# Kernel optimization log

Hardware: AMD Instinct MI355X
Metric: run time of the kernel (lower is better)

The kernel has to match this reference:

```python
import jax, jax.numpy as jnp
import numpy as np

VOCAB, EMB, NDIM, B, T = 50000, 300, 512, 128, 128


def gru_cell(x, h, Wih, Whh, bih, bhh):
    # torch nn.GRU gate order: [r, z, n]
    gi = x @ Wih.T + bih
    gh = h @ Whh.T + bhh
    i_r, i_z, i_n = jnp.split(gi, 3, axis=-1)
    h_r, h_z, h_n = jnp.split(gh, 3, axis=-1)
    r = jax.nn.sigmoid(i_r + h_r)
    z = jax.nn.sigmoid(i_z + h_z)
    n = jnp.tanh(i_n + r * h_n)
    return (1.0 - z) * n + z * h


def masked_gru(X, mask, h0, Wih, Whh, bih, bhh):
    # X: T x B x d, mask: T x B, h0: B x n. Replicates _gru_forward:
    # step-0 output is stored UNmasked (o_tm1 is None), later steps blend.
    h_raw = gru_cell(X[0], h0, Wih, Whh, bih, bhh)
    m0 = mask[0][:, None]
    h = h_raw * m0 + h0 * (1.0 - m0)
    o = h_raw

    def step(carry, inp):
        h, o = carry
        x_t, m_t = inp
        m = m_t[:, None]
        hr = gru_cell(x_t, h, Wih, Whh, bih, bhh)
        h_new = hr * m + h * (1.0 - m)
        o_new = hr * m + o * (1.0 - m)
        return (h_new, o_new), o_new

    (h_f, _), o_rest = jax.lax.scan(step, (h, o), (X[1:], mask[1:]))
    return jnp.concatenate([o[None], o_rest], axis=0), h_f


def rte_forward(premise, hypothesis, E, p_Wih, p_Whh, p_bih, p_bhh,
                h_Wih, h_Whh, h_bih, h_bhh, m_Wih, m_Whh, m_bih, m_bhh,
                W_y, W_h, W_r, W_alpha, out_W, out_b):
    bsz = premise.shape[0]
    n_dim = W_y.shape[0]
    mask_p = (premise != 0).astype(E.dtype).T            # T x B
    mask_h = (hypothesis != 0).astype(E.dtype).T
    enc_p = E[premise].transpose(1, 0, 2)                # T x B x EMB (eval: no dropout)
    enc_h = E[hypothesis].transpose(1, 0, 2)
    h0 = jnp.zeros((bsz, n_dim), dtype=E.dtype)
    o_p, h_n = masked_gru(enc_p, mask_p, h0, p_Wih, p_Whh, p_bih, p_bhh)
    o_h, _ = masked_gru(enc_h, mask_h, h_n, h_Wih, h_Whh, h_bih, h_bhh)

    Y = o_p.transpose(1, 0, 2)                           # B x Tp x n
    Yw = Y @ W_y                                         # hoisted: constant across steps
    maskY = mask_p.T                                     # B x Tp

    def step(r, inp):
        h_t, m_t = inp
        s = h_t @ W_h + r @ W_r                          # B x n
        M = jnp.tanh(Yw + s[:, None, :])                 # B x Tp x n
        alpha = (M @ W_alpha)[..., 0]                    # B x Tp
        alpha = alpha - 1000.0 * (1.0 - maskY)
        alpha = jax.nn.softmax(alpha, axis=-1)
        a = jnp.einsum('bt,btn->bn', alpha, Y)
        m_in = jnp.concatenate([a, h_t], axis=-1)        # B x 2n
        rr = gru_cell(m_in, r, m_Wih, m_Whh, m_bih, m_bhh)
        m = m_t[:, None]
        r_new = rr * m + r * (1.0 - m)
        return r_new, alpha

    r0 = jnp.zeros((bsz, n_dim), dtype=E.dtype)
    r_f, _alpha_vec = jax.lax.scan(step, r0, (o_h, mask_h))
    logits = r_f @ out_W.T + out_b                       # B x 3
    return jax.nn.log_softmax(logits, axis=-1)


def setup_inputs():
    key = jax.random.key(0)
    ks = jax.random.split(key, 22)
    s = 0.05
    def rn(k, sh):
        return jax.random.normal(k, sh, dtype=jnp.float32) * s
    G = 3 * NDIM
    return {
        "premise": jax.random.randint(ks[0], (B, T), 0, VOCAB),
        "hypothesis": jax.random.randint(ks[1], (B, T), 0, VOCAB),
        "E": rn(ks[2], (VOCAB, EMB)),
        "p_Wih": rn(ks[3], (G, EMB)), "p_Whh": rn(ks[4], (G, NDIM)),
        "p_bih": rn(ks[5], (G,)), "p_bhh": rn(ks[6], (G,)),
        "h_Wih": rn(ks[7], (G, EMB)), "h_Whh": rn(ks[8], (G, NDIM)),
        "h_bih": rn(ks[9], (G,)), "h_bhh": rn(ks[10], (G,)),
        "m_Wih": rn(ks[11], (G, 2 * NDIM)), "m_Whh": rn(ks[12], (G, NDIM)),
        "m_bih": rn(ks[13], (G,)), "m_bhh": rn(ks[14], (G,)),
        "W_y": rn(ks[15], (NDIM, NDIM)), "W_h": rn(ks[16], (NDIM, NDIM)),
        "W_r": rn(ks[17], (NDIM, NDIM)), "W_alpha": rn(ks[18], (NDIM, 1)),
        "out_W": rn(ks[19], (3, NDIM)), "out_b": rn(ks[20], (3,)),
    }


def reference(premise, hypothesis, E, p_Wih, p_Whh, p_bih, p_bhh,
              h_Wih, h_Whh, h_bih, h_bhh, m_Wih, m_Whh, m_bih, m_bhh,
              W_y, W_h, W_r, W_alpha, out_W, out_b):
    return rte_forward(premise, hypothesis, E, p_Wih, p_Whh, p_bih, p_bhh,
                       h_Wih, h_Whh, h_bih, h_bhh, m_Wih, m_Whh, m_bih, m_bhh,
                       W_y, W_h, W_r, W_alpha, out_W, out_b)
```

## Files before the change

### kernel.cpp

```cpp
#include <hip/hip_runtime.h>
#include <math.h>

#define B_SZ 128
#define T_SZ 128
#define EMBD 300
#define ND 512
#define G3 1536
#define FPAD 32
#define NFID 320
#define NREP 8

typedef short s16x8 __attribute__((ext_vector_type(8)));
typedef float f32x4 __attribute__((ext_vector_type(4)));
typedef unsigned long long u64;

__device__ __forceinline__ unsigned short f2b(float x) {
    unsigned u = __float_as_uint(x);
    unsigned r = (u + 0x7fff + ((u >> 16) & 1)) >> 16;
    return (unsigned short)r;
}
__device__ __forceinline__ float b2f(unsigned short v) {
    return __uint_as_float(((unsigned)v) << 16);
}
__device__ __forceinline__ float fsigmoid(float x) { return 1.0f / (1.0f + __expf(-x)); }
__device__ __forceinline__ float ftanh(float x) { return 1.0f - 2.0f / (__expf(2.0f * x) + 1.0f); }

__device__ __forceinline__ f32x4 mfma16(s16x8 a, s16x8 b, f32x4 c) {
    return __builtin_amdgcn_mfma_f32_16x16x32_bf16(a, b, c, 0, 0, 0);
}

__device__ __forceinline__ u64 cld64(const void* p) {
    return __hip_atomic_load((const u64*)p, __ATOMIC_RELAXED, __HIP_MEMORY_SCOPE_AGENT);
}
__device__ __forceinline__ void cst64(void* p, u64 v) {
    __hip_atomic_store((u64*)p, v, __ATOMIC_RELAXED, __HIP_MEMORY_SCOPE_AGENT);
}
__device__ __forceinline__ unsigned cld32(const void* p) {
    return __hip_atomic_load((const unsigned*)p, __ATOMIC_RELAXED, __HIP_MEMORY_SCOPE_AGENT);
}
__device__ __forceinline__ void cst32(void* p, unsigned v) {
    __hip_atomic_store((unsigned*)p, v, __ATOMIC_RELAXED, __HIP_MEMORY_SCOPE_AGENT);
}
__device__ __forceinline__ s16x8 cld_frag(const unsigned short* p) {
    union { u64 q[2]; s16x8 v; } u;
    u.q[0] = cld64(p);
    u.q[1] = cld64(p + 4);
    return u.v;
}

__device__ __forceinline__ void postflag(unsigned* flags, int base, int id, unsigned ep)
{
    if (threadIdx.x < NREP)
        cst32(&flags[((long)threadIdx.x * NFID + base + id) * FPAD], ep);
}
__device__ __forceinline__ void waitflags(const unsigned* flags, int base, int n,
                                          unsigned ep, int rep)
{
    const unsigned* fr = flags + (long)rep * NFID * FPAD;
    if (threadIdx.x < 64) {
#pragma unroll 1
        for (int i = threadIdx.x; i < n; i += 64)
            while (cld32(&fr[(long)(base + i) * FPAD]) < ep)
                __builtin_amdgcn_s_sleep(2);
    }
    __syncthreads();
}
__device__ __forceinline__ void fbar(unsigned* flags, int base, int nb, unsigned ep)
{
    __syncthreads();
    postflag(flags, base, blockIdx.x & 63, ep);
    waitflags(flags, base, nb, ep, blockIdx.x & 7);
}

#define FB_GRUP 0
#define FB_GRUH 64
#define FB_LF   128
#define FB_UF   256
#define FB_SF   288

template<typename AT, bool OB>
__global__ __launch_bounds__(256)
void mfma_gemm(const AT* __restrict__ A, const int* __restrict__ idxA,
               const unsigned short* __restrict__ Wb, const float* __restrict__ bias,
               void* __restrict__ Cv,
               int M, int N, int K, int ldA, int Kpad, int ldC, int permC)
{
    __shared__ unsigned short As[64][40];
    __shared__ unsigned short Bs[64][40];
    const int tid = threadIdx.x;
    const int wv = tid >> 6, lane = tid & 63;
    const int wm = wv >> 1, wn = wv & 1;
    const int m0 = blockIdx.y * 64, n0 = blockIdx.x * 64;

    f32x4 acc[2][2] = {{{0.f,0.f,0.f,0.f},{0.f,0.f,0.f,0.f}},
                       {{0.f,0.f,0.f,0.f},{0.f,0.f,0.f,0.f}}};
    const int r_st = tid >> 2, k_st = (tid & 3) * 8;

    long arow = -1;
    {
        int gm = m0 + r_st;
        if (gm < M) arow = idxA ? (long)idxA[gm] : (long)gm;
    }

    const int kIters = (K + 31) / 32;
    for (int it = 0; it < kIters; ++it) {
        const int kg = it * 32 + k_st;
        {
            s16x8 pk = {0,0,0,0,0,0,0,0};
            if (arow >= 0) {
                if constexpr (sizeof(AT) == 2) {
                    if (kg + 8 <= K) {
                        pk = *(const s16x8*)((const unsigned short*)A + arow * (long)ldA + kg);
                    } else {
#pragma unroll
                        for (int j = 0; j < 8; ++j)
                            if (kg + j < K) pk[j] = (short)((const unsigned short*)A)[arow * (long)ldA + kg + j];
                    }
                } else {
                    if (kg + 8 <= K) {
                        const float* p = (const float*)A + arow * (long)ldA + kg;
                        f32x4 u0 = *(const f32x4*)p;
                        f32x4 u1 = *(const f32x4*)(p + 4);
#pragma unroll
                        for (int j = 0; j < 4; ++j) { pk[j] = (short)f2b(u0[j]); pk[4+j] = (short)f2b(u1[j]); }
                    } else {
#pragma unroll
                        for (int j = 0; j < 8; ++j) {
                            int kk = kg + j;
                            if (kk < K) pk[j] = (short)f2b(((const float*)A)[arow * (long)ldA + kk]);
                        }
                    }
                }
            }
            *(s16x8*)&As[r_st][k_st] = pk;
        }
        {
            int gn = n0 + r_st;
            s16x8 pk = {0,0,0,0,0,0,0,0};
            if (gn < N) pk = *(const s16x8*)&Wb[(long)gn * Kpad + kg];
            *(s16x8*)&Bs[r_st][k_st] = pk;
        }
        __syncthreads();
        {
            const int koff = (lane >> 4) * 8;
            s16x8 af[2], bfr[2];
#pragma unroll
            for (int f = 0; f < 2; ++f) {
                af[f]  = *(s16x8*)&As[wm * 32 + f * 16 + (lane & 15)][koff];
                bfr[f] = *(s16x8*)&Bs[wn * 32 + f * 16 + (lane & 15)][koff];
            }
#pragma unroll
            for (int fi = 0; fi < 2; ++fi)
#pragma unroll
                for (int fj = 0; fj < 2; ++fj)
                    acc[fi][fj] = mfma16(af[fi], bfr[fj], acc[fi][fj]);
        }
        __syncthreads();
    }
#pragma unroll
    for (int fi = 0; fi < 2; ++fi)
#pragma unroll
        for (int fj = 0; fj < 2; ++fj)
#pragma unroll
            for (int r = 0; r < 4; ++r) {
                int m = m0 + wm * 32 + fi * 16 + (lane >> 4) * 4 + r;
                int n = n0 + wn * 32 + fj * 16 + (lane & 15);
                if (m < M && n < N) {
                    float v = acc[fi][fj][r];
                    if (bias) v += bias[n];
                    long mo = permC ? ((long)(m & 127) * B_SZ + (m >> 7)) : (long)m;
                    if constexpr (OB) ((unsigned short*)Cv)[mo * ldC + n] = f2b(v);
                    else               ((float*)Cv)[mo * ldC + n] = v;
                }
            }
}

#define GRU_NB 64
__global__ __launch_bounds__(256, 1)
void gru_chain(const unsigned short* __restrict__ Whh_b, const float* __restrict__ GI,
               const float* __restrict__ bhh, const int* __restrict__ toks,
               float* __restrict__ h32,
               unsigned short* __restrict__ h16a, unsigned short* __restrict__ h16b,
               unsigned short* __restrict__ o_bt,
               unsigned* __restrict__ flags, int fbase)
{
    __shared__ unsigned short wlds[3][16][512];
    __shared__ unsigned short ht[64][20];
    const int tid = threadIdx.x;
    const int wv = tid >> 6, lane = tid & 63;
    const int dt = blockIdx.x & 31, bh = blockIdx.x >> 5;
    const int b0 = bh * 64;

    for (int s = 0; s < 12; ++s) {
        int slot = tid + s * 256;
        int g = slot >> 10, rem = slot & 1023, ks = rem >> 6, ln = rem & 63;
        int row = g * ND + dt * 16 + (ln & 15);
        int k = ks * 32 + (ln >> 4) * 8;
        *(s16x8*)&wlds[g][ks][ln * 8] = *(const s16x8*)&Whh_b[(long)row * ND + k];
    }
    __syncthreads();

    const int d = dt * 16 + (lane & 15);
    const int brow = b0 + wv * 16 + (lane >> 4) * 4;
    const int arow = b0 + wv * 16 + (lane & 15);
    const int akoff = (lane >> 4) * 8;

    float hreg[4];
#pragma unroll
    for (int rr = 0; rr < 4; ++rr) hreg[rr] = h32[(long)(brow + rr) * ND + d];

    float o_run[4] = {0.f, 0.f, 0.f, 0.f};
    unsigned ep = 0;

    for (int t = 0; t < T_SZ; ++t) {
        const unsigned short* hin16 = (t & 1) ? h16b : h16a;
        unsigned short* hout16 = (t & 1) ? h16a : h16b;

        const float* git = GI + (long)t * (B_SZ * G3);
        float gi_r[4], gi_z[4], gi_n[4]; int mk[4];
#pragma unroll
        for (int rr = 0; rr < 4; ++rr) {
            int b = brow + rr;
            gi_r[rr] = git[(long)b * G3 + d];
            gi_z[rr] = git[(long)b * G3 + ND + d];
            gi_n[rr] = git[(long)b * G3 + 2 * ND + d];
            mk[rr]   = toks[b * T_SZ + t];
        }

        f32x4 acc0 = {0,0,0,0}, acc1 = {0,0,0,0}, acc2 = {0,0,0,0};
#pragma unroll
        for (int ks = 0; ks < 16; ++ks) {
            s16x8 a  = cld_frag(&hin16[(long)arow * ND + ks * 32 + akoff]);
            s16x8 br = *(s16x8*)&wlds[0][ks][lane * 8];
            s16x8 bz = *(s16x8*)&wlds[1][ks][lane * 8];
            s16x8 bn = *(s16x8*)&wlds[2][ks][lane * 8];
            acc0 = mfma16(a, br, acc0);
            acc1 = mfma16(a, bz, acc1);
            acc2 = mfma16(a, bn, acc2);
        }

#pragma unroll
        for (int rr = 0; rr < 4; ++rr) {
            int b = brow + rr;
            float rg = fsigmoid(gi_r[rr] + acc0[rr] + bhh[d]);
            float zg = fsigmoid(gi_z[rr] + acc1[rr] + bhh[ND + d]);
            float ng = ftanh(gi_n[rr] + rg * (acc2[rr] + bhh[2 * ND + d]));
            float hr = (1.0f - zg) * ng + zg * hreg[rr];
            bool m = mk[rr] != 0;
            float hn = m ? hr : hreg[rr];
            hreg[rr] = hn;
            ht[b - b0][lane & 15] = f2b(hn);
            if (t == T_SZ - 1) h32[(long)b * ND + d] = hn;
            o_run[rr] = (t == 0) ? hr : (m ? hr : o_run[rr]);
            o_bt[((long)b * T_SZ + t) * ND + d] = f2b(o_run[rr]);
        }
        __syncthreads();
        {
            int bl = tid & 63, dq = tid >> 6;
            u64 v = *(u64*)&ht[bl][dq * 4];
            cst64(&hout16[(long)(b0 + bl) * ND + dt * 16 + dq * 4], v);
        }
        fbar(flags, fbase, GRU_NB, ++ep);
    }
}

#define UP_NB 32
#define YPITCH 536
__global__ __launch_bounds__(256, 1)
void match_chain(const unsigned short* __restrict__ WrT_b,
                 const unsigned short* __restrict__ mWihL_b,
                 const unsigned short* __restrict__ mWhh_b,
                 const unsigned short* __restrict__ OHWh_tb,
                 const unsigned short* __restrict__ OHGI_tb,
                 const float* __restrict__ m_bhh, const float* __restrict__ Walpha,
                 const unsigned short* __restrict__ Yw_bb,
                 const unsigned short* __restrict__ Y_bb,
                 const int* __restrict__ prem, const int* __restrict__ hyp,
                 float* __restrict__ r32,
                 unsigned short* __restrict__ r16a, unsigned short* __restrict__ r16b,
                 unsigned short* __restrict__ a16, unsigned short* __restrict__ s16,
                 unsigned* __restrict__ flags)
{
    __shared__ __align__(16) unsigned char smem[157696];
    const int tid = threadIdx.x;
    const int wv = tid >> 6, lane = tid & 63;

    if (blockIdx.x < 128) {
        const int b = blockIdx.x;
        const int rep = b & 7;
        unsigned short (*ywl)[YPITCH] = (unsigned short(*)[YPITCH])smem;
        float* wal  = (float*)(smem + 137216);
        float* sarr = (float*)(smem + 139264);
        float* part = (float*)(smem + 141312);
        float* lg   = (float*)(smem + 142336);
        float* red  = (float*)(smem + 142848);
        float* sr2  = (float*)(smem + 142880);

        for (int s = 0; s < 32; ++s) {
            int c = s * 256 + tid;
            int row = c >> 6, cg = c & 63;
            *(s16x8*)&ywl[row][cg * 8] =
                *(const s16x8*)&Yw_bb[((long)b * T_SZ + row) * ND + cg * 8];
        }
        if (tid < 128) {
            f32x4 w = *(const f32x4*)&Walpha[tid * 4];
            *(f32x4*)&wal[tid * 4] = w;
        }
        float mmreg = 0.f;
        if (tid < 128) mmreg = (prem[b * T_SZ + tid] != 0) ? 0.f : 1000.f;
        __syncthreads();

        const int tp = tid >> 1, gh = tid & 1;
        const unsigned short* yrow = &ywl[tp][gh * 256];
        const float* sp  = &sarr[gh * 256];
        const float* wap = &wal[gh * 256];
        const int g = tid >> 7, lt = tid & 127, n4 = lt * 4;

        for (int t = 0; t < T_SZ; ++t) {
            waitflags(flags, FB_SF, UP_NB, (unsigned)(t + 1), rep);
            if (tid < 64) {
                s16x8 q = cld_frag(&s16[(long)b * ND + tid * 8]);
#pragma unroll
                for (int j = 0; j < 8; ++j) sarr[tid * 8 + j] = b2f((unsigned short)q[j]);
            }
            __syncthreads();
            {
                float acc = 0.f;
#pragma unroll 4
                for (int i8 = 0; i8 < 32; ++i8) {
                    s16x8 yw = *(const s16x8*)&yrow[i8 * 8];
                    f32x4 s0 = *(const f32x4*)&sp[i8 * 8];
                    f32x4 s1 = *(const f32x4*)&sp[i8 * 8 + 4];
                    f32x4 w0 = *(const f32x4*)&wap[i8 * 8];
                    f32x4 w1 = *(const f32x4*)&wap[i8 * 8 + 4];
#pragma unroll
                    for (int j = 0; j < 4; ++j)
                        acc += ftanh(b2f((unsigned short)yw[j]) + s0[j]) * w0[j];
#pragma unroll
                    for (int j = 0; j < 4; ++j)
                        acc += ftanh(b2f((unsigned short)yw[4 + j]) + s1[j]) * w1[j];
                }
                part[tid] = acc;
            }
            __syncthreads();
            if (tid < 128) lg[tid] = __expf(part[tid * 2] + part[tid * 2 + 1] - mmreg);
            __syncthreads();
            float suml = 0.f;
            f32x4 acw = {0.f, 0.f, 0.f, 0.f};
#pragma unroll 8
            for (int i = 0; i < 64; ++i) {
                int tpp = g * 64 + i;
                float al = lg[tpp];
                suml += al;
                u64 q = *(const u64*)&Y_bb[((long)b * T_SZ + tpp) * ND + n4];
                acw[0] += al * b2f((unsigned short)q);
                acw[1] += al * b2f((unsigned short)(q >> 16));
                acw[2] += al * b2f((unsigned short)(q >> 32));
                acw[3] += al * b2f((unsigned short)(q >> 48));
            }
            if (g == 1) {
                *(f32x4*)&sr2[n4] = acw;
                if (lt == 0) red[0] = suml;
            }
            __syncthreads();
            if (g == 0) {
                float inv = 1.0f / (suml + red[0]);
                f32x4 o = *(f32x4*)&sr2[n4];
                u64 pk = (u64)f2b((acw[0] + o[0]) * inv) | ((u64)f2b((acw[1] + o[1]) * inv) << 16)
                       | ((u64)f2b((acw[2] + o[2]) * inv) << 32) | ((u64)f2b((acw[3] + o[3]) * inv) << 48);
                cst64(&a16[(long)b * ND + n4], pk);
            }
            __syncthreads();
            postflag(flags, FB_LF, b, (unsigned)(t + 1));
        }
    } else {
        const int ug = blockIdx.x - 128;
        const int rep = ug & 7;
        unsigned short (*wA)[16][512] = (unsigned short(*)[16][512])smem;
        unsigned short (*wR)[16][512] = (unsigned short(*)[16][512])(smem + 49152);
        float (*bounce)[84] = (float(*)[84])(smem + 49152 + 65536);

        for (int s = 0; s < 12; ++s) {
            int slot = tid + s * 256;
            int fam = slot >> 10, rem = slot & 1023, ks = rem >> 6, ln = rem & 63;
            int row = fam * ND + ug * 16 + (ln & 15);
            int k = ks * 32 + (ln >> 4) * 8;
            *(s16x8*)&wA[fam][ks][ln * 8] = *(const s16x8*)&mWihL_b[(long)row * ND + k];
        }
        for (int s = 0; s < 16; ++s) {
            int slot = tid + s * 256;
            int fam = slot >> 10, rem = slot & 1023, ks = rem >> 6, ln = rem & 63;
            int k = ks * 32 + (ln >> 4) * 8;
            const unsigned short* src = (fam < 3)
                ? &mWhh_b[(long)(fam * ND + ug * 16 + (ln & 15)) * ND + k]
                : &WrT_b[(long)(ug * 16 + (ln & 15)) * ND + k];
            *(s16x8*)&wR[fam][ks][ln * 8] = *(const s16x8*)src;
        }
        __syncthreads();

        const int akoff = (lane >> 4) * 8;
        const int cb = tid >> 1;
        const int half = tid & 1;
        const int d0 = ug * 16 + half * 8;

        f32x4 rpA = {0,0,0,0}, rpB = {0,0,0,0};

        for (int t = 0; t < T_SZ; ++t) {
            const unsigned short* ohw = &OHWh_tb[((long)t * B_SZ + cb) * ND + d0];
            u64 qa = *(const u64*)ohw;
            u64 qb = *(const u64*)(ohw + 4);
            const unsigned short* og = &OHGI_tb[((long)t * B_SZ + cb) * G3];
            u64 q0a = *(const u64*)&og[d0];            u64 q0b = *(const u64*)&og[d0 + 4];
            u64 q1a = *(const u64*)&og[ND + d0];       u64 q1b = *(const u64*)&og[ND + d0 + 4];
            u64 q2a = *(const u64*)&og[2 * ND + d0];   u64 q2b = *(const u64*)&og[2 * ND + d0 + 4];
            int hv = hyp[cb * T_SZ + t];

            waitflags(flags, FB_UF, UP_NB, (unsigned)t, rep);
            const unsigned short* r16rd = (t & 1) ? r16b : r16a;
            unsigned short*       r16wr = (t & 1) ? r16a : r16b;

            f32x4 aSR[2] = {{0,0,0,0},{0,0,0,0}}, aSZ[2] = {{0,0,0,0},{0,0,0,0}};
            f32x4 aHN[2] = {{0,0,0,0},{0,0,0,0}}, aS[2]  = {{0,0,0,0},{0,0,0,0}};
            f32x4 aGN[2] = {{0,0,0,0},{0,0,0,0}};
#pragma unroll
            for (int f = 0; f < 2; ++f) {
                int row = wv * 32 + f * 16 + (lane & 15);
#pragma unroll
                for (int ks = 0; ks < 16; ++ks) {
                    s16x8 a = cld_frag(&r16rd[(long)row * ND + ks * 32 + akoff]);
                    aSR[f] = mfma16(a, *(s16x8*)&wR[0][ks][lane * 8], aSR[f]);
                    aSZ[f] = mfma16(a, *(s16x8*)&wR[1][ks][lane * 8], aSZ[f]);
                    aHN[f] = mfma16(a, *(s16x8*)&wR[2][ks][lane * 8], aHN[f]);
                    aS[f]  = mfma16(a, *(s16x8*)&wR[3][ks][lane * 8], aS[f]);
                }
            }
#pragma unroll
            for (int f = 0; f < 2; ++f)
#pragma unroll
                for (int rr = 0; rr < 4; ++rr)
                    bounce[wv * 32 + f * 16 + (lane >> 4) * 4 + rr][64 + (lane & 15)] = aS[f][rr];
            __syncthreads();
            {
                u64 w0 = 0, w1 = 0;
#pragma unroll
                for (int j = 0; j < 4; ++j) {
                    float v0 = bounce[cb][64 + half * 8 + j]     + b2f((unsigned short)(qa >> (16 * j)));
                    float v1 = bounce[cb][64 + half * 8 + 4 + j] + b2f((unsigned short)(qb >> (16 * j)));
                    w0 |= (u64)f2b(v0) << (16 * j);
                    w1 |= (u64)f2b(v1) << (16 * j);
                }
                cst64(&s16[(long)cb * ND + d0], w0);
                cst64(&s16[(long)cb * ND + d0 + 4], w1);
            }
            __syncthreads();
            postflag(flags, FB_SF, ug, (unsigned)(t + 1));

            waitflags(flags, FB_LF, 128, (unsigned)(t + 1), rep);
#pragma unroll
            for (int f = 0; f < 2; ++f) {
                int row = wv * 32 + f * 16 + (lane & 15);
#pragma unroll
                for (int ks = 0; ks < 16; ++ks) {
                    s16x8 a = cld_frag(&a16[(long)row * ND + ks * 32 + akoff]);
                    aSR[f] = mfma16(a, *(s16x8*)&wA[0][ks][lane * 8], aSR[f]);
                    aSZ[f] = mfma16(a, *(s16x8*)&wA[1][ks][lane * 8], aSZ[f]);
                    aGN[f] = mfma16(a, *(s16x8*)&wA[2][ks][lane * 8], aGN[f]);
                }
            }
#pragma unroll
            for (int f = 0; f < 2; ++f)
#pragma unroll
                for (int rr = 0; rr < 4; ++rr) {
                    int bb = wv * 32 + f * 16 + (lane >> 4) * 4 + rr;
                    bounce[bb][0  + (lane & 15)] = aSR[f][rr];
                    bounce[bb][16 + (lane & 15)] = aSZ[f][rr];
                    bounce[bb][32 + (lane & 15)] = aGN[f][rr];
                    bounce[bb][48 + (lane & 15)] = aHN[f][rr];
                }
            __syncthreads();
            {
                bool mkk = hv != 0;
                u64 w0 = 0, w1 = 0;
#pragma unroll
                for (int j = 0; j < 8; ++j) {
                    int dl = half * 8 + j;
                    int dd = ug * 16 + dl;
                    u64 qg0 = (j < 4) ? q0a : q0b;
                    u64 qg1 = (j < 4) ? q1a : q1b;
                    u64 qg2 = (j < 4) ? q2a : q2b;
                    int sh = 16 * (j & 3);
                    float sr  = bounce[cb][0 + dl]  + b2f((unsigned short)(qg0 >> sh)) + m_bhh[dd];
                    float sz  = bounce[cb][16 + dl] + b2f((unsigned short)(qg1 >> sh)) + m_bhh[ND + dd];
                    float gin = bounce[cb][32 + dl] + b2f((unsigned short)(qg2 >> sh));
                    float ghn = bounce[cb][48 + dl] + m_bhh[2 * ND + dd];
                    float rg = fsigmoid(sr), zg = fsigmoid(sz);
                    float ng = ftanh(gin + rg * ghn);
                    float rp = (j < 4) ? rpA[j & 3] : rpB[j & 3];
                    float rn = (1.0f - zg) * ng + zg * rp;
                    float v = mkk ? rn : rp;
                    if (j < 4) rpA[j & 3] = v; else rpB[j & 3] = v;
                    if (j < 4) w0 |= (u64)f2b(v) << sh; else w1 |= (u64)f2b(v) << sh;
                }
                if (t == T_SZ - 1) {
                    *(f32x4*)&r32[(long)cb * ND + d0] = rpA;
                    *(f32x4*)&r32[(long)cb * ND + d0 + 4] = rpB;
                }
                cst64(&r16wr[(long)cb * ND + d0], w0);
                cst64(&r16wr[(long)cb * ND + d0 + 4], w1);
            }
            __syncthreads();
            postflag(flags, FB_UF, ug, (unsigned)(t + 1));
        }
    }
}

__global__ void prep_idx(const int* __restrict__ prem, const int* __restrict__ hyp,
                         int* __restrict__ idx_p, int* __restrict__ idx_h)
{
    int i = blockIdx.x * blockDim.x + threadIdx.x;
    if (i < B_SZ * T_SZ) {
        int t = i / B_SZ, b = i % B_SZ;
        idx_p[i] = prem[b * T_SZ + t];
        idx_h[i] = hyp[b * T_SZ + t];
    }
}

__global__ void conv_w(const float* __restrict__ in, unsigned short* __restrict__ out,
                       int N, int K, int Kpad, int ldIn, int colOff)
{
    long i = (long)blockIdx.x * blockDim.x + threadIdx.x;
    if (i >= (long)N * Kpad) return;
    int n = (int)(i / Kpad), k = (int)(i % Kpad);
    float v = (k < K) ? in[(long)n * ldIn + k + colOff] : 0.0f;
    out[i] = f2b(v);
}

__global__ void conv_wT(const float* __restrict__ in, unsigned short* __restrict__ out,
                        int N, int K, int Kpad, int ldIn)
{
    long i = (long)blockIdx.x * blockDim.x + threadIdx.x;
    if (i >= (long)N * Kpad) return;
    int n = (int)(i / Kpad), k = (int)(i % Kpad);
    float v = (k < K) ? in[(long)k * ldIn + n] : 0.0f;
    out[i] = f2b(v);
}

__global__ void zero_kernel(float* __restrict__ p, int n)
{
    int i = blockIdx.x * blockDim.x + threadIdx.x;
    if (i < n) p[i] = 0.0f;
}

__global__ void final_logits(const float* __restrict__ r, const float* __restrict__ outW,
                             const float* __restrict__ outb, float* __restrict__ out)
{
    int b = blockIdx.x;
    int lane = threadIdx.x;
    float a0 = 0.0f, a1 = 0.0f, a2 = 0.0f;
    for (int k = lane; k < ND; k += 64) {
        float rv = r[(long)b * ND + k];
        a0 += rv * outW[0 * ND + k];
        a1 += rv * outW[1 * ND + k];
        a2 += rv * outW[2 * ND + k];
    }
#pragma unroll
    for (int off = 32; off; off >>= 1) {
        a0 += __shfl_down(a0, off);
        a1 += __shfl_down(a1, off);
        a2 += __shfl_down(a2, off);
    }
    if (lane == 0) {
        float l0 = a0 + outb[0], l1 = a1 + outb[1], l2 = a2 + outb[2];
        float mx = fmaxf(l0, fmaxf(l1, l2));
        float se = expf(l0 - mx) + expf(l1 - mx) + expf(l2 - mx);
        float ls = mx + logf(se);
        out[b * 3 + 0] = l0 - ls;
        out[b * 3 + 1] = l1 - ls;
        out[b * 3 + 2] = l2 - ls;
    }
}

extern "C" void kernel_launch(void* const* d_in, const int* in_sizes, int n_in,
                              void* d_out, int out_size, void* d_ws, size_t ws_size,
                              hipStream_t stream)
{
    const int*   prem    = (const int*)d_in[0];
    const int*   hyp     = (const int*)d_in[1];
    const float* E       = (const float*)d_in[2];
    const float* p_Wih   = (const float*)d_in[3];
    const float* p_Whh   = (const float*)d_in[4];
    const float* p_bih   = (const float*)d_in[5];
    const float* p_bhh   = (const float*)d_in[6];
    const float* h_Wih   = (const float*)d_in[7];
    const float* h_Whh   = (const float*)d_in[8];
    const float* h_bih   = (const float*)d_in[9];
    const float* h_bhh   = (const float*)d_in[10];
    const float* m_Wih   = (const float*)d_in[11];
    const float* m_Whh   = (const float*)d_in[12];
    const float* m_bih   = (const float*)d_in[13];
    const float* m_bhh   = (const float*)d_in[14];
    const float* W_y     = (const float*)d_in[15];
    const float* W_h     = (const float*)d_in[16];
    const float* W_r     = (const float*)d_in[17];
    const float* W_alpha = (const float*)d_in[18];
    const float* out_W   = (const float*)d_in[19];
    const float* out_b   = (const float*)d_in[20];
    float* out = (float*)d_out;

    const int MB = T_SZ * B_SZ;
    const int NFLAGS = NREP * NFID * FPAD;

    float* ws = (float*)d_ws;
    size_t off = 0;
    float* GI    = ws + off; off += (size_t)MB * G3;
    float* h32   = ws + off; off += (size_t)B_SZ * ND;
    float* r32   = ws + off; off += (size_t)B_SZ * ND;
    unsigned* flags = (unsigned*)(ws + off); off += NFLAGS;
    int* idx_p = (int*)(ws + off); off += (size_t)B_SZ * T_SZ;
    int* idx_h = (int*)(ws + off); off += (size_t)B_SZ * T_SZ;
    unsigned short* ub = (unsigned short*)(ws + off);
    size_t uoff = 0;
    unsigned short* o_p_bt = ub + uoff; uoff += (size_t)MB * ND;
    unsigned short* o_h_bt = ub + uoff; uoff += (size_t)MB * ND;
    unsigned short* Yw_bb  = ub + uoff; uoff += (size_t)MB * ND;
    unsigned short* OHWh_tb= ub + uoff; uoff += (size_t)MB * ND;
    unsigned short* OHGI_tb= ub + uoff; uoff += (size_t)MB * G3;
    unsigned short* h16a   = ub + uoff; uoff += (size_t)B_SZ * ND;
    unsigned short* h16b   = ub + uoff; uoff += (size_t)B_SZ * ND;
    unsigned short* r16a   = ub + uoff; uoff += (size_t)B_SZ * ND;
    unsigned short* r16b   = ub + uoff; uoff += (size_t)B_SZ * ND;
    unsigned short* a16    = ub + uoff; uoff += (size_t)B_SZ * ND;
    unsigned short* s16    = ub + uoff; uoff += (size_t)B_SZ * ND;
    unsigned short* pWih_b = ub + uoff; uoff += (size_t)G3 * 320;
    unsigned short* hWih_b = ub + uoff; uoff += (size_t)G3 * 320;
    unsigned short* pWhh_b = ub + uoff; uoff += (size_t)G3 * ND;
    unsigned short* hWhh_b = ub + uoff; uoff += (size_t)G3 * ND;
    unsigned short* mWihL_b= ub + uoff; uoff += (size_t)G3 * ND;
    unsigned short* mWihR  = ub + uoff; uoff += (size_t)G3 * ND;
    unsigned short* mWhh_b = ub + uoff; uoff += (size_t)G3 * ND;
    unsigned short* WyT_b  = ub + uoff; uoff += (size_t)ND * ND;
    unsigned short* WhT_b  = ub + uoff; uoff += (size_t)ND * ND;
    unsigned short* WrT_b  = ub + uoff; uoff += (size_t)ND * ND;
    off += (uoff + 1) / 2;
    if (ws_size < off * sizeof(float)) return;

    auto cblk = [](long n) { return (int)((n + 255) / 256); };

    prep_idx<<<cblk(MB), 256, 0, stream>>>(prem, hyp, idx_p, idx_h);
    conv_w <<<cblk((long)G3 * 320), 256, 0, stream>>>(p_Wih, pWih_b, G3, EMBD, 320, EMBD, 0);
    conv_w <<<cblk((long)G3 * 320), 256, 0, stream>>>(h_Wih, hWih_b, G3, EMBD, 320, EMBD, 0);
    conv_w <<<cblk((long)G3 * ND), 256, 0, stream>>>(p_Whh, pWhh_b, G3, ND, ND, ND, 0);
    conv_w <<<cblk((long)G3 * ND), 256, 0, stream>>>(h_Whh, hWhh_b, G3, ND, ND, ND, 0);
    conv_w <<<cblk((long)G3 * ND), 256, 0, stream>>>(m_Wih, mWihL_b, G3, ND, ND, 2 * ND, 0);
    conv_w <<<cblk((long)G3 * ND), 256, 0, stream>>>(m_Wih, mWihR, G3, ND, ND, 2 * ND, ND);
    conv_w <<<cblk((long)G3 * ND), 256, 0, stream>>>(m_Whh, mWhh_b, G3, ND, ND, ND, 0);
    conv_wT<<<cblk((long)ND * ND), 256, 0, stream>>>(W_y, WyT_b, ND, ND, ND, ND);
    conv_wT<<<cblk((long)ND * ND), 256, 0, stream>>>(W_h, WhT_b, ND, ND, ND, ND);
    conv_wT<<<cblk((long)ND * ND), 256, 0, stream>>>(W_r, WrT_b, ND, ND, ND, ND);
    zero_kernel<<<cblk(B_SZ * ND), 256, 0, stream>>>(h32, B_SZ * ND);
    zero_kernel<<<cblk(B_SZ * ND / 2), 256, 0, stream>>>((float*)h16a, B_SZ * ND / 2);
    zero_kernel<<<cblk(B_SZ * ND), 256, 0, stream>>>(r32, B_SZ * ND);
    zero_kernel<<<cblk(B_SZ * ND / 2), 256, 0, stream>>>((float*)r16a, B_SZ * ND / 2);
    zero_kernel<<<cblk(B_SZ * ND / 2), 256, 0, stream>>>((float*)r16b, B_SZ * ND / 2);
    zero_kernel<<<cblk(NFLAGS), 256, 0, stream>>>((float*)flags, NFLAGS);

    {
        dim3 g(G3 / 64, MB / 64);
        mfma_gemm<float, false><<<g, 256, 0, stream>>>(E, idx_p, pWih_b, p_bih, GI,
                                                       MB, G3, EMBD, EMBD, 320, G3, 0);
    }
    gru_chain<<<GRU_NB, 256, 0, stream>>>(pWhh_b, GI, p_bhh, prem, h32, h16a, h16b,
                                          o_p_bt, flags, FB_GRUP);

    {
        dim3 g(G3 / 64, MB / 64);
        mfma_gemm<float, false><<<g, 256, 0, stream>>>(E, idx_h, hWih_b, h_bih, GI,
                                                       MB, G3, EMBD, EMBD, 320, G3, 0);
    }
    gru_chain<<<GRU_NB, 256, 0, stream>>>(hWhh_b, GI, h_bhh, hyp, h32, h16a, h16b,
                                          o_h_bt, flags, FB_GRUH);

    {
        dim3 g(ND / 64, MB / 64);
        mfma_gemm<unsigned short, true><<<g, 256, 0, stream>>>(o_p_bt, nullptr, WyT_b, nullptr,
                                                               Yw_bb, MB, ND, ND, ND, ND, ND, 0);
        mfma_gemm<unsigned short, true><<<g, 256, 0, stream>>>(o_h_bt, nullptr, WhT_b, nullptr,
                                                               OHWh_tb, MB, ND, ND, ND, ND, ND, 1);
        dim3 g2(G3 / 64, MB / 64);
        mfma_gemm<unsigned short, true><<<g2, 256, 0, stream>>>(o_h_bt, nullptr, mWihR, m_bih,
                                                                OHGI_tb, MB, G3, ND, ND, ND, G3, 1);
    }

    match_chain<<<160, 256, 0, stream>>>(WrT_b, mWihL_b, mWhh_b, OHWh_tb, OHGI_tb,
                                         m_bhh, W_alpha, Yw_bb, o_p_bt, prem, hyp,
                                         r32, r16a, r16b, a16, s16, flags);

    final_logits<<<B_SZ, 64, 0, stream>>>(r32, out_W, out_b, out);
}
```

Baseline: 7.025 ms.

## Store recurrent hidden/attention vectors in MFMA-fragment order for contiguous loads

The bf16 hidden-state buffers exchanged between blocks each step (GRU h, attention output a16, match r16) are now written in a pre-swizzled MFMA fragment layout. Each lane's A-fragment load becomes one contiguous 512-element chunk per (row-group, k-step) instead of strided row reads. This is meant to cut the latency of the coherent global loads on the serial recurrence critical path. Writers must compute the swizzled addresses, and every consumer must agree on the new layout. Any reader that still expects row-major order would break.

```diff
diff --git a/kernel.cpp b/kernel.cpp
--- a/kernel.cpp
+++ b/kernel.cpp
@@ -202,8 +202,12 @@
 
     const int d = dt * 16 + (lane & 15);
     const int brow = b0 + wv * 16 + (lane >> 4) * 4;
-    const int arow = b0 + wv * 16 + (lane & 15);
-    const int akoff = (lane >> 4) * 8;
+    const long fhrd = ((long)(bh * 4 + wv) * 16) << 9;
+
+    const int bl = tid & 63, dq = tid >> 6;
+    const long fhwr = (((long)(bh * 4 + (bl >> 4)) * 16 + (dt >> 1)) << 9)
+                    + (((((dt & 1) * 16 + dq * 4) >> 3) * 16 + (bl & 15)) * 8)
+                    + (((dt & 1) * 16 + dq * 4) & 7);
 
     float hreg[4];
 #pragma unroll
@@ -230,7 +234,7 @@
         f32x4 acc0 = {0,0,0,0}, acc1 = {0,0,0,0}, acc2 = {0,0,0,0};
 #pragma unroll
         for (int ks = 0; ks < 16; ++ks) {
-            s16x8 a  = cld_frag(&hin16[(long)arow * ND + ks * 32 + akoff]);
+            s16x8 a  = cld_frag(&hin16[fhrd + ((long)ks << 9) + lane * 8]);
             s16x8 br = *(s16x8*)&wlds[0][ks][lane * 8];
             s16x8 bz = *(s16x8*)&wlds[1][ks][lane * 8];
             s16x8 bn = *(s16x8*)&wlds[2][ks][lane * 8];
@@ -256,9 +260,8 @@
         }
         __syncthreads();
         {
-            int bl = tid & 63, dq = tid >> 6;
             u64 v = *(u64*)&ht[bl][dq * 4];
-            cst64(&hout16[(long)(b0 + bl) * ND + dt * 16 + dq * 4], v);
+            cst64(&hout16[fhwr], v);
         }
         fbar(flags, fbase, GRU_NB, ++ep);
     }
@@ -315,6 +318,8 @@
         const float* sp  = &sarr[gh * 256];
         const float* wap = &wal[gh * 256];
         const int g = tid >> 7, lt = tid & 127, n4 = lt * 4;
+        const long fa_wr = (((long)(b >> 4) * 16 + (n4 >> 5)) << 9)
+                         + ((((n4 >> 3) & 3) * 16 + (b & 15)) * 8) + (n4 & 7);
 
         for (int t = 0; t < T_SZ; ++t) {
             waitflags(flags, FB_SF, UP_NB, (unsigned)(t + 1), rep);
@@ -368,7 +373,7 @@
                 f32x4 o = *(f32x4*)&sr2[n4];
                 u64 pk = (u64)f2b((acw[0] + o[0]) * inv) | ((u64)f2b((acw[1] + o[1]) * inv) << 16)
                        | ((u64)f2b((acw[2] + o[2]) * inv) << 32) | ((u64)f2b((acw[3] + o[3]) * inv) << 48);
-                cst64(&a16[(long)b * ND + n4], pk);
+                cst64(&a16[fa_wr], pk);
             }
             __syncthreads();
             postflag(flags, FB_LF, b, (unsigned)(t + 1));
@@ -398,10 +403,11 @@
         }
         __syncthreads();
 
-        const int akoff = (lane >> 4) * 8;
         const int cb = tid >> 1;
         const int half = tid & 1;
         const int d0 = ug * 16 + half * 8;
+        const long fr_wr = (((long)(cb >> 4) * 16 + (ug >> 1)) << 9)
+                         + ((((d0 >> 3) & 3) * 16 + (cb & 15)) * 8);
 
         f32x4 rpA = {0,0,0,0}, rpB = {0,0,0,0};
 
@@ -424,10 +430,10 @@
             f32x4 aGN[2] = {{0,0,0,0},{0,0,0,0}};
 #pragma unroll
             for (int f = 0; f < 2; ++f) {
-                int row = wv * 32 + f * 16 + (lane & 15);
+                const long gbase = ((long)(wv * 2 + f) * 16) << 9;
 #pragma unroll
                 for (int ks = 0; ks < 16; ++ks) {
-                    s16x8 a = cld_frag(&r16rd[(long)row * ND + ks * 32 + akoff]);
+                    s16x8 a = cld_frag(&r16rd[gbase + ((long)ks << 9) + lane * 8]);
                     aSR[f] = mfma16(a, *(s16x8*)&wR[0][ks][lane * 8], aSR[f]);
                     aSZ[f] = mfma16(a, *(s16x8*)&wR[1][ks][lane * 8], aSZ[f]);
                     aHN[f] = mfma16(a, *(s16x8*)&wR[2][ks][lane * 8], aHN[f]);
@@ -458,10 +464,10 @@
             waitflags(flags, FB_LF, 128, (unsigned)(t + 1), rep);
 #pragma unroll
             for (int f = 0; f < 2; ++f) {
-                int row = wv * 32 + f * 16 + (lane & 15);
+                const long gbase = ((long)(wv * 2 + f) * 16) << 9;
 #pragma unroll
                 for (int ks = 0; ks < 16; ++ks) {
-                    s16x8 a = cld_frag(&a16[(long)row * ND + ks * 32 + akoff]);
+                    s16x8 a = cld_frag(&a16[gbase + ((long)ks << 9) + lane * 8]);
                     aSR[f] = mfma16(a, *(s16x8*)&wA[0][ks][lane * 8], aSR[f]);
                     aSZ[f] = mfma16(a, *(s16x8*)&wA[1][ks][lane * 8], aSZ[f]);
                     aGN[f] = mfma16(a, *(s16x8*)&wA[2][ks][lane * 8], aGN[f]);
@@ -505,8 +511,8 @@
                     *(f32x4*)&r32[(long)cb * ND + d0] = rpA;
                     *(f32x4*)&r32[(long)cb * ND + d0 + 4] = rpB;
                 }
-                cst64(&r16wr[(long)cb * ND + d0], w0);
-                cst64(&r16wr[(long)cb * ND + d0 + 4], w1);
+                cst64(&r16wr[fr_wr], w0);
+                cst64(&r16wr[fr_wr + 4], w1);
             }
             __syncthreads();
             postflag(flags, FB_UF, ug, (unsigned)(t + 1));
```

After: 6.666 ms. 1.05x faster.
